# Performance work log

Hardware: AMD Instinct MI355X
Metric: run time of the kernel (lower is better)

## Reference

```python
import jax, jax.numpy as jnp
import numpy as np

B, C, V = 64, 8, 4096
V2 = V // 4
K = 8
CL1, CL2 = 32, 64
FC1, FC2 = 512, 2
DEG = 32
BN_EPS = 1e-5


def setup_inputs() -> dict:
    key = jax.random.key(0)
    ks = jax.random.split(key, 12)
    x = jax.random.normal(ks[0], (B, C, V), dtype=jnp.float32)
    E1, E2 = V * DEG, V2 * DEG
    # fixed out-degree COO sparse rescaled Laplacians; values scaled by 1/deg so
    # spectral radius ~<= 1 and the Chebyshev recursion stays bounded
    rows1 = jnp.repeat(jnp.arange(V, dtype=jnp.int32), DEG)
    cols1 = jax.random.randint(ks[1], (E1,), 0, V, dtype=jnp.int32)
    vals1 = jax.random.uniform(ks[2], (E1,), minval=-1.0, maxval=1.0, dtype=jnp.float32) / DEG
    rows2 = jnp.repeat(jnp.arange(V2, dtype=jnp.int32), DEG)
    cols2 = jax.random.randint(ks[3], (E2,), 0, V2, dtype=jnp.int32)
    vals2 = jax.random.uniform(ks[4], (E2,), minval=-1.0, maxval=1.0, dtype=jnp.float32) / DEG
    # Glorot-ish scales as in original init (scale = sqrt(2/(Fin+Fout)))
    s1 = float(np.sqrt(2.0 / (C * K + CL1)))
    w1 = jax.random.uniform(ks[5], (CL1, C * K), minval=-s1, maxval=s1, dtype=jnp.float32)
    b1 = jnp.zeros((CL1,), jnp.float32)
    s2 = float(np.sqrt(2.0 / (CL1 * K + CL2)))
    w2 = jax.random.uniform(ks[6], (CL2, CL1 * K), minval=-s2, maxval=s2, dtype=jnp.float32)
    b2 = jnp.zeros((CL2,), jnp.float32)
    FC1_IN = CL2 * V // 16
    s3 = float(np.sqrt(2.0 / (FC1_IN + FC1)))
    fc1_w = jax.random.uniform(ks[7], (FC1, FC1_IN), minval=-s3, maxval=s3, dtype=jnp.float32)
    fc1_b = jnp.zeros((FC1,), jnp.float32)
    s4 = float(np.sqrt(2.0 / (FC1 + FC2)))
    fc2_w = jax.random.uniform(ks[8], (FC2, FC1), minval=-s4, maxval=s4, dtype=jnp.float32)
    fc2_b = jnp.zeros((FC2,), jnp.float32)
    return {"x": x, "rows1": rows1, "cols1": cols1, "vals1": vals1,
            "rows2": rows2, "cols2": cols2, "vals2": vals2,
            "w1": w1, "b1": b1, "w2": w2, "b2": b2,
            "fc1_w": fc1_w, "fc1_b": fc1_b, "fc2_w": fc2_w, "fc2_b": fc2_b}


def _spmm(rows, cols, vals, m, n_rows):
    # sparse (n x n) @ dense (n x F) via gather + segment-sum (rows are sorted)
    return jax.ops.segment_sum(vals[:, None] * m[cols], rows,
                               num_segments=n_rows, indices_are_sorted=True)


def _graph_conv(x, rows, cols, vals, k_size, W, b):
    # x: (B, Cin, V) -> Chebyshev features -> (B, Cout, V)
    Bn, Cin, Vn = x.shape
    x0 = jnp.transpose(x, (2, 1, 0)).reshape(Vn, Cin * Bn)  # (V, C*B)
    xs = [x0]
    if k_size > 1:
        xs.append(_spmm(rows, cols, vals, x0, Vn))
    for _ in range(2, k_size):
        xs.append(2.0 * _spmm(rows, cols, vals, xs[-1]) if False else 2.0 * _spmm(rows, cols, vals, xs[-1], Vn) - xs[-2])
    xk = jnp.stack(xs, axis=0)                              # (K, V, C*B)
    xk = xk.reshape(k_size, Vn, Cin, Bn)
    xk = jnp.transpose(xk, (3, 1, 2, 0)).reshape(Bn * Vn, Cin * k_size)
    out = xk @ W.T + b                                      # (B*V, Cout)
    return jnp.transpose(out.reshape(Bn, Vn, -1), (0, 2, 1))


def _maxpool4(x):
    Bn, Cn, Vn = x.shape
    return x.reshape(Bn, Cn, Vn // 4, 4).max(axis=-1)


def reference(x, rows1, cols1, vals1, rows2, cols2, vals2,
              w1, b1, w2, b2, fc1_w, fc1_b, fc2_w, fc2_b):
    # BatchNorm1d(affine=False), training-mode batch stats over (B, V) per channel
    mean = x.mean(axis=(0, 2), keepdims=True)
    var = x.var(axis=(0, 2), keepdims=True)
    h = (x - mean) / jnp.sqrt(var + BN_EPS)
    h = jax.nn.relu(_graph_conv(h, rows1, cols1, vals1, K, w1, b1))   # (B, 32, 4096)
    h = _maxpool4(h)                                                  # (B, 32, 1024)
    h = jax.nn.relu(_graph_conv(h, rows2, cols2, vals2, K, w2, b2))   # (B, 64, 1024)
    h = _maxpool4(h)                                                  # (B, 64, 256)
    h = h.reshape(h.shape[0], -1)                                     # (B, 16384)
    h = jax.nn.sigmoid(h @ fc1_w.T + fc1_b)                           # dropout = identity (eval)
    return h @ fc2_w.T + fc2_b                                        # (B, 2)
```

## Files before the change

### kernel.cpp

```cpp
#include <hip/hip_runtime.h>
#include <math.h>

#define Bn   64
#define Cin0 8
#define Vn   4096
#define V2n  1024
#define KK   8
#define DEG  32
#define FC1N 512
#define FC1IN 16384
#define BN_EPS 1e-5f

typedef float f32x4 __attribute__((ext_vector_type(4)));

struct Ptr8 { const float* p[8]; };

__global__ void bn_stats_kernel(const float* __restrict__ x, float* __restrict__ stats) {
    int c = blockIdx.x;
    int chunk = blockIdx.y;
    const int per = (Bn * Vn) / 16;
    int base = chunk * per;
    float s = 0.f, s2 = 0.f;
    for (int i = threadIdx.x; i < per; i += 256) {
        int p = base + i;
        int b = p >> 12;
        int v = p & 4095;
        float val = x[((size_t)b * Cin0 + c) * Vn + v];
        s += val; s2 += val * val;
    }
    __shared__ float r1[256], r2[256];
    r1[threadIdx.x] = s; r2[threadIdx.x] = s2;
    __syncthreads();
    for (int off = 128; off > 0; off >>= 1) {
        if (threadIdx.x < off) {
            r1[threadIdx.x] += r1[threadIdx.x + off];
            r2[threadIdx.x] += r2[threadIdx.x + off];
        }
        __syncthreads();
    }
    if (threadIdx.x == 0) {
        atomicAdd(&stats[c], r1[0]);
        atomicAdd(&stats[8 + c], r2[0]);
    }
}

__global__ void bn_apply_t_kernel(const float* __restrict__ x, const float* __restrict__ stats,
                                  float* __restrict__ x0) {
    int c = blockIdx.y;
    int v0 = blockIdx.x * 64;
    const float invN = 1.0f / (float)(Bn * Vn);
    float mean = stats[c] * invN;
    float var  = stats[8 + c] * invN - mean * mean;
    float sc = rsqrtf(var + BN_EPS);
    __shared__ float tile[64][65];
    int tx = threadIdx.x & 63;
    int ty = threadIdx.x >> 6;
    #pragma unroll
    for (int i = 0; i < 16; i++) {
        int b = i * 4 + ty;
        tile[b][tx] = x[((size_t)b * Cin0 + c) * Vn + v0 + tx];
    }
    __syncthreads();
    #pragma unroll
    for (int i = 0; i < 16; i++) {
        int vl = i * 4 + ty;
        float val = (tile[tx][vl] - mean) * sc;
        x0[(size_t)(v0 + vl) * 512 + c * 64 + tx] = val;
    }
}

template <int SLICES>
__global__ __launch_bounds__(256, 4) void spmm_kernel(
    const float* __restrict__ xin, const int* __restrict__ cols,
    const float* __restrict__ vals, const float* __restrict__ prev,
    float* __restrict__ y) {
    constexpr int F = SLICES * 128;
    int id = blockIdx.x;
    int s, g;
    if (SLICES == 4) {
        int xc = id & 7; s = xc >> 1; g = ((id >> 3) << 1) | (xc & 1);
    } else {
        int xc = id & 7; int q = id >> 3; s = (xc << 1) | (q & 1); g = q >> 1;
    }
    int r    = threadIdx.x >> 5;
    int lane = threadIdx.x & 31;
    int v = g * 8 + r;
    int fbase = s * 128 + lane * 4;
    __shared__ int   cs[8][DEG];
    __shared__ float vsh[8][DEG];
    {
        int e = threadIdx.x;
        int vv = g * 8 + (e >> 5);
        cs[e >> 5][e & 31]  = cols[vv * DEG + (e & 31)];
        vsh[e >> 5][e & 31] = vals[vv * DEG + (e & 31)];
    }
    __syncthreads();
    float4 acc = make_float4(0.f, 0.f, 0.f, 0.f);
    #pragma unroll 8
    for (int e = 0; e < DEG; e++) {
        const float4 xv = *(const float4*)(xin + (size_t)cs[r][e] * F + fbase);
        float w = vsh[r][e];
        acc.x += w * xv.x; acc.y += w * xv.y; acc.z += w * xv.z; acc.w += w * xv.w;
    }
    size_t oi = (size_t)v * F + fbase;
    float4 o;
    if (prev) {
        const float4 pv = *(const float4*)(prev + oi);
        o.x = 2.f * acc.x - pv.x; o.y = 2.f * acc.y - pv.y;
        o.z = 2.f * acc.z - pv.z; o.w = 2.f * acc.w - pv.w;
    } else {
        o = acc;
    }
    *(float4*)(y + oi) = o;
}

template <int CIN, int MODE, int NT>
__global__ __launch_bounds__(NT, 2) void gemm_pool_kernel(
    Ptr8 xs, const float* __restrict__ W,
    const float* __restrict__ bias, float* __restrict__ out) {
    constexpr int IN  = CIN * KK;
    constexpr int F   = CIN * 64;
    constexpr int CCH = (MODE == 0) ? 4 : 8;
    constexpr int NCH = CIN / CCH;
    __shared__ float lds[32 * CCH * 64];
    int b  = threadIdx.x & 63;
    int jg = __builtin_amdgcn_readfirstlane(threadIdx.x >> 6);
    int vp = blockIdx.x;
    float acc[4][8] = {};
    for (int ch = 0; ch < NCH; ch++) {
        int c0 = ch * CCH;
        __syncthreads();
        constexpr int NF4 = 32 * CCH * 16;
        for (int i = threadIdx.x; i < NF4; i += NT) {
            int seg = i / (CCH * 16);
            int o4  = i - seg * (CCH * 16);
            int k = seg >> 2, vl = seg & 3;
            const float* gp = xs.p[k] + (size_t)(vp * 4 + vl) * F + c0 * 64 + o4 * 4;
            *(f32x4*)&lds[seg * (CCH * 64) + o4 * 4] = *(const f32x4*)gp;
        }
        __syncthreads();
        for (int cc = 0; cc < CCH; cc++) {
            float xv[8][4];
            #pragma unroll
            for (int k = 0; k < 8; k++)
                #pragma unroll
                for (int vl = 0; vl < 4; vl++)
                    xv[k][vl] = lds[((k * 4 + vl) * CCH + cc) * 64 + b];
            int c = c0 + cc;
            #pragma unroll
            for (int jj = 0; jj < 8; jj++) {
                const float* __restrict__ wr = W + (size_t)(jg * 8 + jj) * IN + c * 8;
                #pragma unroll
                for (int k = 0; k < 8; k++) {
                    float w = wr[k];
                    acc[0][jj] += xv[k][0] * w;
                    acc[1][jj] += xv[k][1] * w;
                    acc[2][jj] += xv[k][2] * w;
                    acc[3][jj] += xv[k][3] * w;
                }
            }
        }
    }
    #pragma unroll
    for (int jj = 0; jj < 8; jj++) {
        int j = jg * 8 + jj;
        float m0 = fmaxf(fmaxf(acc[0][jj], acc[1][jj]), fmaxf(acc[2][jj], acc[3][jj]));
        m0 = fmaxf(m0 + bias[j], 0.0f);
        if (MODE == 0)
            out[((size_t)vp * 32 + j) * 64 + b] = m0;
        else
            out[((size_t)j * 256 + vp) * 64 + b] = m0;
    }
}

__global__ __launch_bounds__(256, 2) void fc1_partial_kernel(
    const float* __restrict__ A,
    const float* __restrict__ Wfc,
    float* __restrict__ part) {
    __shared__ float Alds[128 * 64];
    __shared__ float Wlds[32 * 128];
    int n0 = blockIdx.x * 32;
    int m0 = blockIdx.y * 512;
    int b  = threadIdx.x & 63;
    int ng = threadIdx.x >> 6;
    float acc[8] = {};
    for (int ch = 0; ch < 4; ch++) {
        int mb = m0 + ch * 128;
        __syncthreads();
        {
            const f32x4* __restrict__ src = (const f32x4*)(A + (size_t)mb * 64);
            f32x4* dst = (f32x4*)Alds;
            #pragma unroll
            for (int u = 0; u < 8; u++)
                dst[u * 256 + threadIdx.x] = src[u * 256 + threadIdx.x];
        }
        {
            int r = threadIdx.x >> 3;
            int c4 = (threadIdx.x & 7) * 4;
            const float* __restrict__ wr = Wfc + (size_t)(n0 + r) * FC1IN + mb;
            f32x4* dst = (f32x4*)&Wlds[r * 128];
            #pragma unroll
            for (int u = 0; u < 4; u++)
                dst[c4 + u] = *(const f32x4*)(wr + (c4 + u) * 4);
        }
        __syncthreads();
        for (int mm = 0; mm < 128; mm += 4) {
            float a0 = Alds[(mm + 0) * 64 + b];
            float a1 = Alds[(mm + 1) * 64 + b];
            float a2 = Alds[(mm + 2) * 64 + b];
            float a3 = Alds[(mm + 3) * 64 + b];
            #pragma unroll
            for (int jn = 0; jn < 8; jn++) {
                f32x4 w = *(const f32x4*)&Wlds[(ng * 8 + jn) * 128 + mm];
                acc[jn] += a0 * w.x + a1 * w.y + a2 * w.z + a3 * w.w;
            }
        }
    }
    #pragma unroll
    for (int jn = 0; jn < 8; jn++)
        part[((size_t)blockIdx.y * FC1N + n0 + ng * 8 + jn) * 64 + b] = acc[jn];
}

__global__ void fc1_reduce_kernel(const float* __restrict__ part, const float* __restrict__ bias,
                                  float* __restrict__ outA) {
    int idx = blockIdx.x * 256 + threadIdx.x;
    int n = idx >> 6;
    float s = bias[n];
    #pragma unroll 8
    for (int mc = 0; mc < 32; mc++) s += part[(size_t)mc * 32768 + idx];
    outA[idx] = 1.0f / (1.0f + expf(-s));
}

__global__ __launch_bounds__(1024) void fc2_kernel(const float* __restrict__ Afc,
                                                   const float* __restrict__ W,
                                                   const float* __restrict__ bias,
                                                   float* __restrict__ out) {
    __shared__ float Wl[1024];
    __shared__ float red[1024];
    int t = threadIdx.x;
    Wl[t] = W[t];
    __syncthreads();
    int b = t & 63, o = (t >> 6) & 1, chunk = t >> 7;
    const float* __restrict__ Ap = Afc + (size_t)(chunk * 64) * 64 + b;
    const float* __restrict__ Wp = Wl + o * 512 + chunk * 64;
    float s = 0.f;
    #pragma unroll
    for (int i = 0; i < 64; i++)
        s += Ap[i * 64] * Wp[i];
    red[t] = s;
    __syncthreads();
    if (t < 128) {
        float acc = 0.f;
        #pragma unroll
        for (int c = 0; c < 8; c++) acc += red[c * 128 + t];
        out[(t & 63) * 2 + (t >> 6)] = acc + bias[t >> 6];
    }
}

extern "C" void kernel_launch(void* const* d_in, const int* in_sizes, int n_in,
                              void* d_out, int out_size, void* d_ws, size_t ws_size,
                              hipStream_t stream) {
    const float* x     = (const float*)d_in[0];
    const int*   cols1 = (const int*)  d_in[2];
    const float* vals1 = (const float*)d_in[3];
    const int*   cols2 = (const int*)  d_in[5];
    const float* vals2 = (const float*)d_in[6];
    const float* w1    = (const float*)d_in[7];
    const float* b1    = (const float*)d_in[8];
    const float* w2    = (const float*)d_in[9];
    const float* b2    = (const float*)d_in[10];
    const float* fc1w  = (const float*)d_in[11];
    const float* fc1b  = (const float*)d_in[12];
    const float* fc2w  = (const float*)d_in[13];
    const float* fc2b  = (const float*)d_in[14];

    float* ws = (float*)d_ws;
    const size_t SLOT = (size_t)Vn * 512;
    float* stats = ws;
    float* xs    = ws + 64;
    float* x02   = xs + 8 * SLOT;
    float* h2pT  = x02 + SLOT;
    float* fc1p  = xs;
    float* fc1o  = xs + SLOT;

    (void)hipMemsetAsync(stats, 0, 16 * sizeof(float), stream);
    bn_stats_kernel<<<dim3(8, 16), 256, 0, stream>>>(x, stats);
    bn_apply_t_kernel<<<dim3(64, 8), 256, 0, stream>>>(x, stats, xs);

    for (int k = 1; k < 8; k++)
        spmm_kernel<4><<<dim3(2048), 256, 0, stream>>>(
            xs + (size_t)(k - 1) * SLOT, cols1, vals1,
            (k >= 2) ? xs + (size_t)(k - 2) * SLOT : nullptr,
            xs + (size_t)k * SLOT);
    Ptr8 p1;
    for (int k = 0; k < 8; k++) p1.p[k] = xs + (size_t)k * SLOT;
    gemm_pool_kernel<8, 0, 256><<<dim3(1024), 256, 0, stream>>>(p1, w1, b1, x02);

    Ptr8 p2;
    p2.p[0] = x02;
    for (int k = 1; k < 8; k++) p2.p[k] = xs + (size_t)(k - 1) * SLOT;
    for (int k = 1; k < 8; k++)
        spmm_kernel<16><<<dim3(2048), 256, 0, stream>>>(
            p2.p[k - 1], cols2, vals2,
            (k >= 2) ? p2.p[k - 2] : nullptr,
            (float*)p2.p[k]);
    gemm_pool_kernel<32, 1, 512><<<dim3(256), 512, 0, stream>>>(p2, w2, b2, h2pT);

    fc1_partial_kernel<<<dim3(16, 32), 256, 0, stream>>>(h2pT, fc1w, fc1p);
    fc1_reduce_kernel<<<dim3(128), 256, 0, stream>>>(fc1p, fc1b, fc1o);
    fc2_kernel<<<dim3(1), 1024, 0, stream>>>(fc1o, fc2w, fc2b, (float*)d_out);
}
```

Baseline: 414.5 us.

## Double-buffer gemm_pool input tiles and stage weights in LDS

```diff
diff --git a/kernel.cpp b/kernel.cpp
--- a/kernel.cpp
+++ b/kernel.cpp
@@ -115,50 +115,73 @@
 }
 
 template <int CIN, int MODE, int NT>
-__global__ __launch_bounds__(NT, 2) void gemm_pool_kernel(
+__global__ __launch_bounds__(NT, 1) void gemm_pool_kernel(
     Ptr8 xs, const float* __restrict__ W,
     const float* __restrict__ bias, float* __restrict__ out) {
     constexpr int IN  = CIN * KK;
     constexpr int F   = CIN * 64;
-    constexpr int CCH = (MODE == 0) ? 4 : 8;
+    constexpr int JT  = (MODE == 0) ? 32 : 64;
+    constexpr int CCH = 4;
     constexpr int NCH = CIN / CCH;
-    __shared__ float lds[32 * CCH * 64];
+    constexpr int NF4 = 32 * CCH * 16;
+    constexpr int NL  = NF4 / NT;
+    __shared__ float Wl[JT * IN];
+    __shared__ float buf[2][32 * CCH * 64];
     int b  = threadIdx.x & 63;
     int jg = __builtin_amdgcn_readfirstlane(threadIdx.x >> 6);
     int vp = blockIdx.x;
-    float acc[4][8] = {};
-    for (int ch = 0; ch < NCH; ch++) {
+    for (int i = threadIdx.x; i < JT * IN / 4; i += NT)
+        ((f32x4*)Wl)[i] = ((const f32x4*)W)[i];
+    f32x4 regs[NL];
+    auto LOADREG = [&](int ch) {
         int c0 = ch * CCH;
-        __syncthreads();
-        constexpr int NF4 = 32 * CCH * 16;
-        for (int i = threadIdx.x; i < NF4; i += NT) {
+        #pragma unroll
+        for (int u = 0; u < NL; u++) {
+            int i  = u * NT + threadIdx.x;
             int seg = i / (CCH * 16);
             int o4  = i - seg * (CCH * 16);
             int k = seg >> 2, vl = seg & 3;
-            const float* gp = xs.p[k] + (size_t)(vp * 4 + vl) * F + c0 * 64 + o4 * 4;
-            *(f32x4*)&lds[seg * (CCH * 64) + o4 * 4] = *(const f32x4*)gp;
-        }
-        __syncthreads();
+            regs[u] = *(const f32x4*)(xs.p[k] + (size_t)(vp * 4 + vl) * F + c0 * 64 + o4 * 4);
+        }
+    };
+    auto WRITELDS = [&](int bi) {
+        #pragma unroll
+        for (int u = 0; u < NL; u++) {
+            int i  = u * NT + threadIdx.x;
+            int seg = i / (CCH * 16);
+            int o4  = i - seg * (CCH * 16);
+            *(f32x4*)&buf[bi][seg * (CCH * 64) + o4 * 4] = regs[u];
+        }
+    };
+    float acc[4][8] = {};
+    LOADREG(0);
+    WRITELDS(0);
+    __syncthreads();
+    for (int ch = 0; ch < NCH; ch++) {
+        if (ch + 1 < NCH) LOADREG(ch + 1);
+        const float* __restrict__ bp = buf[ch & 1];
+        #pragma unroll
         for (int cc = 0; cc < CCH; cc++) {
             float xv[8][4];
             #pragma unroll
             for (int k = 0; k < 8; k++)
                 #pragma unroll
                 for (int vl = 0; vl < 4; vl++)
-                    xv[k][vl] = lds[((k * 4 + vl) * CCH + cc) * 64 + b];
-            int c = c0 + cc;
+                    xv[k][vl] = bp[((k * 4 + vl) * CCH + cc) * 64 + b];
+            int c = ch * CCH + cc;
             #pragma unroll
             for (int jj = 0; jj < 8; jj++) {
-                const float* __restrict__ wr = W + (size_t)(jg * 8 + jj) * IN + c * 8;
+                f32x4 w0 = *(const f32x4*)&Wl[(jg * 8 + jj) * IN + c * 8];
+                f32x4 w1 = *(const f32x4*)&Wl[(jg * 8 + jj) * IN + c * 8 + 4];
                 #pragma unroll
-                for (int k = 0; k < 8; k++) {
-                    float w = wr[k];
-                    acc[0][jj] += xv[k][0] * w;
-                    acc[1][jj] += xv[k][1] * w;
-                    acc[2][jj] += xv[k][2] * w;
-                    acc[3][jj] += xv[k][3] * w;
-                }
+                for (int vl = 0; vl < 4; vl++)
+                    acc[vl][jj] += xv[0][vl] * w0.x + xv[1][vl] * w0.y + xv[2][vl] * w0.z + xv[3][vl] * w0.w
+                                 + xv[4][vl] * w1.x + xv[5][vl] * w1.y + xv[6][vl] * w1.z + xv[7][vl] * w1.w;
             }
+        }
+        if (ch + 1 < NCH) {
+            WRITELDS((ch + 1) & 1);
+            __syncthreads();
         }
     }
     #pragma unroll
```

New measurement: 1.499 ms. +261.7%, slower.
